# Kernel optimization log

Hardware: AMD Instinct MI355X
Metric: run time of the kernel (lower is better)

## Reference

```python
import math
import jax, jax.numpy as jnp
import numpy as np

N_HEADS = 16
NUM_BUCKETS = 32
MAX_DISTANCE = 128
ROTARY_BASE = 10000.0


def rotate_half(x):
    x1, x2 = jnp.split(x, 2, axis=-1)
    return jnp.concatenate((-x2, x1), axis=-1)


def rotary_freqs(T, dim):
    inv_freq = 1.0 / (ROTARY_BASE ** (jnp.arange(0, dim, 2, dtype=jnp.float32) / dim))
    t = jnp.arange(T, dtype=jnp.float32)
    freqs = jnp.einsum('i,j->ij', t, inv_freq)  # [T, dim/2]
    return jnp.concatenate((freqs, freqs), axis=-1)  # [T, dim]


def rel_pos_bucket_causal(rel_pos, num_buckets=NUM_BUCKETS, max_distance=MAX_DISTANCE):
    n = jnp.maximum(-rel_pos, 0)  # [T, T] int
    max_exact = num_buckets // 2
    is_small = n < max_exact
    n_safe = jnp.maximum(n, 1).astype(jnp.float32)
    val_if_large = max_exact + (
        jnp.log(n_safe / max_exact) / math.log(max_distance / max_exact) * (num_buckets - max_exact)
    ).astype(jnp.int32)
    val_if_large = jnp.minimum(val_if_large, num_buckets - 1)
    return jnp.where(is_small, n, val_if_large)


def setup_inputs() -> dict:
    key = jax.random.key(0)
    ks = jax.random.split(key, 10)
    B, T, C = 2, 2048, 1024
    s = 0.02
    return {
        'x':  jax.random.normal(ks[0], (B, T, C), dtype=jnp.float32),
        'Wq': jax.random.normal(ks[1], (C, C), dtype=jnp.float32) * s,
        'bq': jnp.zeros((C,), dtype=jnp.float32),
        'Wk': jax.random.normal(ks[2], (C, C), dtype=jnp.float32) * s,
        'bk': jnp.zeros((C,), dtype=jnp.float32),
        'Wv': jax.random.normal(ks[3], (C, C), dtype=jnp.float32) * s,
        'bv': jnp.zeros((C,), dtype=jnp.float32),
        'Wp': jax.random.normal(ks[4], (C, C), dtype=jnp.float32) * s,
        'bp': jnp.zeros((C,), dtype=jnp.float32),
        'rel_bias_table': jax.random.normal(ks[5], (NUM_BUCKETS, N_HEADS), dtype=jnp.float32) * s,
    }


def reference(x, Wq, bq, Wk, bk, Wv, bv, Wp, bp, rel_bias_table):
    B, T, C = x.shape
    H = N_HEADS
    D = C // H

    def heads(y):
        return y.reshape(B, T, H, D).transpose(0, 2, 1, 3)  # [B,H,T,D]

    q = heads(x @ Wq + bq)
    k = heads(x @ Wk + bk)
    v = heads(x @ Wv + bv)

    # rotary (use_xpos=False -> scale=1)
    freqs = rotary_freqs(T, D)  # [T, D]
    cos, sin = jnp.cos(freqs), jnp.sin(freqs)
    q = q * cos + rotate_half(q) * sin
    k = k * cos + rotate_half(k) * sin

    # relative position bias (causal, scale=1.0)
    pos = jnp.arange(T)
    rel_pos = pos[None, :] - pos[:, None]  # k_pos - q_pos
    bucket = rel_pos_bucket_causal(rel_pos)  # [T, T]
    bias = rel_bias_table[bucket]  # [T, T, H]
    bias = bias.transpose(2, 0, 1)  # [H, T, T]

    att = jnp.einsum('bhid,bhjd->bhij', q, k) + bias[None]
    att = att * (1.0 / math.sqrt(D))
    causal = pos[None, :] <= pos[:, None]  # tril mask [T, T]
    att = jnp.where(causal[None, None], att, -jnp.inf)
    att = jax.nn.softmax(att, axis=-1)

    y = jnp.einsum('bhij,bhjd->bhid', att, v)  # [B,H,T,D]
    y = y.transpose(0, 2, 1, 3).reshape(B, T, C)
    return y @ Wp + bp
```

## Files before the change

kernel.cpp:

```cpp
#include <hip/hip_runtime.h>
#include <hip/hip_bf16.h>
#include <math.h>

#define B_ 2
#define T_ 2048
#define C_ 1024
#define H_ 16
#define D_ 64
#define M_ (B_ * T_)
#define K_ 1024

#define SCALE2 0.18033688011112043f

typedef short bf16x8 __attribute__((ext_vector_type(8)));
typedef float f32x4  __attribute__((ext_vector_type(4)));
typedef unsigned int u32;

__device__ __forceinline__ float u2f(unsigned short u) {
    union { unsigned int i; float f; } v; v.i = ((unsigned int)u) << 16; return v.f;
}
__device__ __forceinline__ unsigned short f2b(float f) {
    __hip_bfloat16 h = __float2bfloat16(f);
    return *reinterpret_cast<unsigned short*>(&h);
}
__device__ __forceinline__ u32 pack_bf16_rnd(float a, float b) {
    const u32 au = __float_as_uint(a) + 0x8000u;
    const u32 bu = __float_as_uint(b) + 0x8000u;
    return __builtin_amdgcn_perm(bu, au, 0x07060302u);
}
__device__ __forceinline__ void load_lds16(const void* g, void* l) {
    __builtin_amdgcn_global_load_lds(
        (const __attribute__((address_space(1))) u32*)g,
        (__attribute__((address_space(3))) u32*)l, 16, 0, 0);
}

__global__ __launch_bounds__(256) void prep(
    const float* __restrict__ x,
    const float* __restrict__ W0, const float* __restrict__ W1,
    const float* __restrict__ W2, const float* __restrict__ W3,
    const float* __restrict__ tbl,
    unsigned short* __restrict__ xb,
    unsigned short* __restrict__ T0, unsigned short* __restrict__ T1,
    unsigned short* __restrict__ T2, unsigned short* __restrict__ T3,
    float* __restrict__ dtab, float2* __restrict__ trig)
{
    __shared__ __align__(16) unsigned short tile[64][72];
    const int bx = blockIdx.x;
    const int tid = threadIdx.x;

    if (bx < 2048) {
        const int idx = bx * 256 + tid;
        const float4 a = reinterpret_cast<const float4*>(x)[idx * 2];
        const float4 b = reinterpret_cast<const float4*>(x)[idx * 2 + 1];
        unsigned short t[8] = {f2b(a.x), f2b(a.y), f2b(a.z), f2b(a.w),
                               f2b(b.x), f2b(b.y), f2b(b.z), f2b(b.w)};
        reinterpret_cast<bf16x8*>(xb)[idx] = *reinterpret_cast<const bf16x8*>(t);
    } else if (bx < 3072) {
        const int w = bx - 2048;
        const int z = w >> 8;
        const int rem = w & 255;
        const int k0 = (rem & 15) * 64, n0 = (rem >> 4) * 64;
        const float* W = z == 0 ? W0 : z == 1 ? W1 : z == 2 ? W2 : W3;
        unsigned short* Wt = z == 0 ? T0 : z == 1 ? T1 : z == 2 ? T2 : T3;

        #pragma unroll
        for (int it = 0; it < 4; ++it) {
            const int idx = it * 256 + tid;
            const int r = idx >> 4, c = (idx & 15) * 4;
            const float4 w4 = *reinterpret_cast<const float4*>(W + (size_t)(k0 + r) * C_ + n0 + c);
            tile[r][c + 0] = f2b(w4.x); tile[r][c + 1] = f2b(w4.y);
            tile[r][c + 2] = f2b(w4.z); tile[r][c + 3] = f2b(w4.w);
        }
        __syncthreads();
        #pragma unroll
        for (int it = 0; it < 2; ++it) {
            const int idx = it * 256 + tid;
            const int nc = idx >> 3, kc = (idx & 7) * 8;
            unsigned short tmp[8];
            #pragma unroll
            for (int e = 0; e < 8; ++e) tmp[e] = tile[kc + e][nc];
            *reinterpret_cast<bf16x8*>(Wt + (size_t)(n0 + nc) * K_ + k0 + kc) =
                *reinterpret_cast<const bf16x8*>(tmp);
        }
    } else {
        const int idx = (bx - 3072) * 256 + tid;
        if (idx < H_ * T_) {
            const int h = idx >> 11, n = idx & (T_ - 1);
            int bucket;
            if (n < 16) bucket = n;
            else {
                int vb = 16 + (int)(log2f((float)n * 0.0625f) * (16.0f / 3.0f));
                bucket = vb < 31 ? vb : 31;
            }
            dtab[idx] = tbl[bucket * H_ + h] * SCALE2;
        }
        const int t = idx >> 5, j = idx & 31;
        const float inv = exp2f(-(float)j * (13.287712379549449f / 32.0f));
        const float ang = (float)t * inv;
        trig[idx] = make_float2(cosf(ang), sinf(ang));
    }
}

template<int BN>
__device__ __forceinline__ void gemm_core(
    const unsigned short* __restrict__ A, const unsigned short* __restrict__ Bt,
    const float* __restrict__ bias, const float2* __restrict__ trig,
    float rot_scale, float* __restrict__ outf,
    unsigned short* __restrict__ outb, int mode, int m0, int n0)
{
    constexpr int FN  = BN / 32;
    constexpr int BCH = BN / 64;
    constexpr int NLD = 2 + BCH;
    __shared__ __align__(16) unsigned short As0[128 * 32];
    __shared__ __align__(16) unsigned short As1[128 * 32];
    __shared__ __align__(16) unsigned short As2[128 * 32];
    __shared__ __align__(16) unsigned short Bs0[BN * 32];
    __shared__ __align__(16) unsigned short Bs1[BN * 32];
    __shared__ __align__(16) unsigned short Bs2[BN * 32];

    const int tid = threadIdx.x;
    const int wid = tid >> 6, lane = tid & 63;
    const int l16 = lane & 15, quad = lane >> 4;
    const int wm = wid >> 1, wn = wid & 1;

    f32x4 acc[4][FN];
    #pragma unroll
    for (int i = 0; i < 4; ++i)
        #pragma unroll
        for (int j = 0; j < FN; ++j) acc[i][j] = (f32x4){0.f, 0.f, 0.f, 0.f};

    auto stage = [&](unsigned short* Asb, unsigned short* Bsb, int k0) {
        #pragma unroll
        for (int it = 0; it < 2; ++it) {
            const int idx = it * 256 + tid;
            const int row = idx >> 2, ch = (idx & 3) * 8;
            load_lds16(A + (size_t)(m0 + row) * K_ + k0 + ch,
                       (char*)Asb + it * 4096 + wid * 1024);
        }
        #pragma unroll
        for (int it = 0; it < BCH; ++it) {
            const int idx = it * 256 + tid;
            const int row = idx >> 2, ch = (idx & 3) * 8;
            load_lds16(Bt + (size_t)(n0 + row) * K_ + k0 + ch,
                       (char*)Bsb + it * 4096 + wid * 1024);
        }
    };
    auto compute = [&](const unsigned short* Asb, const unsigned short* Bsb) {
        bf16x8 af[4], bf[FN];
        #pragma unroll
        for (int i = 0; i < 4; ++i)
            af[i] = *reinterpret_cast<const bf16x8*>(&Asb[(wm * 64 + i * 16 + l16) * 32 + quad * 8]);
        #pragma unroll
        for (int j = 0; j < FN; ++j)
            bf[j] = *reinterpret_cast<const bf16x8*>(&Bsb[(wn * (BN / 2) + j * 16 + l16) * 32 + quad * 8]);
        #pragma unroll
        for (int i = 0; i < 4; ++i)
            #pragma unroll
            for (int j = 0; j < FN; ++j)
                acc[i][j] = __builtin_amdgcn_mfma_f32_16x16x32_bf16(af[i], bf[j], acc[i][j], 0, 0, 0);
    };
    auto step = [&](const unsigned short* cA, const unsigned short* cB,
                    unsigned short* nA, unsigned short* nB, int kn, bool do_stage) {
        if constexpr (NLD == 4) asm volatile("s_waitcnt vmcnt(4)" ::: "memory");
        else                    asm volatile("s_waitcnt vmcnt(3)" ::: "memory");
        __builtin_amdgcn_s_barrier();
        __builtin_amdgcn_sched_barrier(0);
        if (do_stage) stage(nA, nB, kn);
        compute(cA, cB);
    };

    stage(As0, Bs0, 0);
    stage(As1, Bs1, 32);

    for (int kb = 0; kb < 30; kb += 3) {
        step(As0, Bs0, As2, Bs2, (kb + 2) * 32, true);
        step(As1, Bs1, As0, Bs0, (kb + 3) * 32, true);
        step(As2, Bs2, As1, Bs1, (kb + 4) * 32, true);
    }
    step(As0, Bs0, As2, Bs2, 0, false);
    asm volatile("s_waitcnt vmcnt(0)" ::: "memory");
    __builtin_amdgcn_s_barrier();
    __builtin_amdgcn_sched_barrier(0);
    compute(As1, Bs1);

    if (mode == 1) {
        #pragma unroll
        for (int i = 0; i < 4; ++i) {
            const int mb = m0 + wm * 64 + i * 16 + quad * 4;
            const int bb = mb >> 11, tb = mb & (T_ - 1);
            #pragma unroll
            for (int jc = 0; jc < FN / 2; ++jc) {
                const int n_lo = n0 + wn * (BN / 2) + jc * 16 + l16;
                const int h = n_lo >> 6, d = n_lo & 63;
                const float bv_lo = bias[n_lo], bv_hi = bias[n_lo + 32];
                unsigned short* po = outb + (((size_t)bb * H_ + h) * T_ + tb) * D_ + d;
                #pragma unroll
                for (int r = 0; r < 4; ++r) {
                    const float2 cs = trig[(tb + r) * 32 + d];
                    const float a = acc[i][jc][r] + bv_lo;
                    const float b = acc[i][jc + FN / 2][r] + bv_hi;
                    po[(size_t)r * D_]      = f2b((a * cs.x - b * cs.y) * rot_scale);
                    po[(size_t)r * D_ + 32] = f2b((b * cs.x + a * cs.y) * rot_scale);
                }
            }
        }
        return;
    }

    #pragma unroll
    for (int i = 0; i < 4; ++i) {
        const int mb = m0 + wm * 64 + i * 16 + quad * 4;
        #pragma unroll
        for (int j = 0; j < FN; ++j) {
            const int n = n0 + wn * (BN / 2) + j * 16 + l16;
            const float bv = bias[n];
            if (mode == 2) {
                const int bb = mb >> 11, t = mb & (T_ - 1);
                const int h = n >> 6, d = n & 63;
                uint2 w;
                w.x = pack_bf16_rnd(acc[i][j][0] + bv, acc[i][j][1] + bv);
                w.y = pack_bf16_rnd(acc[i][j][2] + bv, acc[i][j][3] + bv);
                *reinterpret_cast<uint2*>(
                    outb + (((size_t)bb * H_ + h) * D_ + d) * T_ + t) = w;
            } else {
                #pragma unroll
                for (int r = 0; r < 4; ++r)
                    outf[(size_t)(mb + r) * C_ + n] = acc[i][j][r] + bv;
            }
        }
    }
}

__global__ __launch_bounds__(256) void gemm_qkv(
    const unsigned short* __restrict__ A,
    const unsigned short* __restrict__ Wq, const unsigned short* __restrict__ Wk,
    const unsigned short* __restrict__ Wv,
    const float* __restrict__ bq, const float* __restrict__ bk,
    const float* __restrict__ bv, const float2* __restrict__ trig,
    unsigned short* __restrict__ Qo, unsigned short* __restrict__ Ko,
    unsigned short* __restrict__ Vto)
{
    const int lin = (int)blockIdx.x;
    const int g = lin & 7, slot = lin >> 3;
    const int w = g * 96 + slot;
    const int z = w >> 8, rem = w & 255;
    const int m0 = (rem >> 3) * 128, n0 = (rem & 7) * 128;

    const unsigned short* Bt = z == 0 ? Wq : z == 1 ? Wk : Wv;
    const float* bias = z == 0 ? bq : z == 1 ? bk : bv;
    unsigned short* outb = z == 0 ? Qo : z == 1 ? Ko : Vto;
    const float rs = z == 0 ? SCALE2 : 1.0f;
    gemm_core<128>(A, Bt, bias, trig, rs, nullptr, outb, z == 2 ? 2 : 1, m0, n0);
}

__global__ __launch_bounds__(256) void gemm_proj(
    const unsigned short* __restrict__ A, const unsigned short* __restrict__ Bt,
    const float* __restrict__ bias, float* __restrict__ outf)
{
    const int lin = (int)blockIdx.x;
    const int g = lin & 7, slot = lin >> 3;
    const int w = g * 64 + slot;
    const int m0 = (w >> 4) * 128, n0 = (w & 15) * 64;
    gemm_core<64>(A, Bt, bias, nullptr, 1.0f, outf, nullptr, 0, m0, n0);
}

__global__ __launch_bounds__(256) void flash_attn(
    const unsigned short* __restrict__ Q, const unsigned short* __restrict__ K,
    const unsigned short* __restrict__ Vt, const float* __restrict__ dtab,
    unsigned short* __restrict__ Y)
{
    __shared__ __align__(16) unsigned short Ks[2][64][72];
    __shared__ __align__(16) unsigned short Vs[2][64][72];
    __shared__ __align__(16) unsigned short Ps[4][16][72];
    __shared__ __align__(16) float bias_ls[64 + T_];

    const int lin = (int)(blockIdx.y * gridDim.x + blockIdx.x);
    const int bh  = lin & 31;
    const int rem = lin >> 5;
    const int h = bh & (H_ - 1), b = bh >> 4;
    const int tid = threadIdx.x;
    const int wid = tid >> 6, lane = tid & 63;
    const int l16 = lane & 15, quad = lane >> 4;
    const size_t base = (size_t)bh * T_ * D_;
    const size_t vbase = (size_t)bh * D_ * T_;

    const int qta = (rem + bh) & 15;
    const int qtb = 31 - qta;

    if (tid < 64) bias_ls[tid] = -INFINITY;
    for (int ii = tid; ii < qtb * 64 + 64; ii += 256) bias_ls[64 + ii] = dtab[h * T_ + ii];

    bf16x8 ones;
    #pragma unroll
    for (int e = 0; e < 8; ++e) ones[e] = (short)0x3F80;

    const int sr0 = tid >> 3,         sch0 = (tid & 7) * 8;
    const int sr1 = (tid + 256) >> 3, sch1 = ((tid + 256) & 7) * 8;

    bf16x8 kr[2], vr[2];
    kr[0] = *reinterpret_cast<const bf16x8*>(K + base + (size_t)sr0 * D_ + sch0);
    kr[1] = *reinterpret_cast<const bf16x8*>(K + base + (size_t)sr1 * D_ + sch1);
    vr[0] = *reinterpret_cast<const bf16x8*>(Vt + vbase + (size_t)sr0 * T_ + sch0);
    vr[1] = *reinterpret_cast<const bf16x8*>(Vt + vbase + (size_t)sr1 * T_ + sch1);
    *reinterpret_cast<bf16x8*>(&Ks[0][sr0][sch0]) = kr[0];
    *reinterpret_cast<bf16x8*>(&Ks[0][sr1][sch1]) = kr[1];
    *reinterpret_cast<bf16x8*>(&Vs[0][sr0][sch0]) = vr[0];
    *reinterpret_cast<bf16x8*>(&Vs[0][sr1][sch1]) = vr[1];
    kr[0] = *reinterpret_cast<const bf16x8*>(K + base + (size_t)(64 + sr0) * D_ + sch0);
    kr[1] = *reinterpret_cast<const bf16x8*>(K + base + (size_t)(64 + sr1) * D_ + sch1);
    vr[0] = *reinterpret_cast<const bf16x8*>(Vt + vbase + (size_t)sr0 * T_ + 64 + sch0);
    vr[1] = *reinterpret_cast<const bf16x8*>(Vt + vbase + (size_t)sr1 * T_ + 64 + sch1);
    __syncthreads();

    int t = 0;
    for (int qi = 0; qi < 2; ++qi) {
        const int qt = qi ? qta : qtb;
        const int q0 = qt * 64;
        const int arow = q0 + wid * 16 + l16;
        const int crow = q0 + wid * 16 + quad * 4;
        const int nbase = crow - l16 * 4;

        bf16x8 qf[2];
        qf[0] = *reinterpret_cast<const bf16x8*>(Q + base + (size_t)arow * D_ + quad * 8);
        qf[1] = *reinterpret_cast<const bf16x8*>(Q + base + (size_t)arow * D_ + 32 + quad * 8);

        f32x4 o[4], ol;
        #pragma unroll
        for (int c = 0; c < 4; ++c) o[c] = (f32x4){0.f, 0.f, 0.f, 0.f};
        ol = (f32x4){0.f, 0.f, 0.f, 0.f};

        for (int kt = 0; kt <= qt; ++kt, ++t) {
            const int j0 = kt * 64;
            const int cur = t & 1, nxt = cur ^ 1;

            if (t < 32) {
                *reinterpret_cast<bf16x8*>(&Ks[nxt][sr0][sch0]) = kr[0];
                *reinterpret_cast<bf16x8*>(&Ks[nxt][sr1][sch1]) = kr[1];
                *reinterpret_cast<bf16x8*>(&Vs[nxt][sr0][sch0]) = vr[0];
                *reinterpret_cast<bf16x8*>(&Vs[nxt][sr1][sch1]) = vr[1];
            }
            if (t < 31) {
                const int tn = t + 2;
                const int jn = (tn <= qtb ? tn : tn - qtb - 1) * 64;
                kr[0] = *reinterpret_cast<const bf16x8*>(K + base + (size_t)(jn + sr0) * D_ + sch0);
                kr[1] = *reinterpret_cast<const bf16x8*>(K + base + (size_t)(jn + sr1) * D_ + sch1);
                vr[0] = *reinterpret_cast<const bf16x8*>(Vt + vbase + (size_t)sr0 * T_ + jn + sch0);
                vr[1] = *reinterpret_cast<const bf16x8*>(Vt + vbase + (size_t)sr1 * T_ + jn + sch1);
            }

            const int d0 = nbase - j0;
            const f32x4 blo = *reinterpret_cast<const f32x4*>(&bias_ls[60 + d0]);
            const f32x4 bhi = *reinterpret_cast<const f32x4*>(&bias_ls[64 + d0]);

            f32x4 sc[4];
            #pragma unroll
            for (int c = 0; c < 4; ++c) {
                #pragma unroll
                for (int r = 0; r < 4; ++r)
                    sc[c][r] = (r >= c) ? bhi[r - c] : blo[4 + r - c];
            }
            __builtin_amdgcn_s_setprio(1);
            #pragma unroll
            for (int c = 0; c < 4; ++c) {
                #pragma unroll
                for (int s = 0; s < 2; ++s) {
                    bf16x8 kf = *reinterpret_cast<const bf16x8*>(
                        &Ks[cur][l16 * 4 + c][s * 32 + quad * 8]);
                    sc[c] = __builtin_amdgcn_mfma_f32_16x16x32_bf16(qf[s], kf, sc[c], 0, 0, 0);
                }
            }
            __builtin_amdgcn_s_setprio(0);

            #pragma unroll
            for (int r = 0; r < 4; ++r) {
                const float p0 = __builtin_amdgcn_exp2f(sc[0][r]);
                const float p1 = __builtin_amdgcn_exp2f(sc[1][r]);
                const float p2 = __builtin_amdgcn_exp2f(sc[2][r]);
                const float p3 = __builtin_amdgcn_exp2f(sc[3][r]);
                uint2 w;
                w.x = pack_bf16_rnd(p0, p1);
                w.y = pack_bf16_rnd(p2, p3);
                *reinterpret_cast<uint2*>(&Ps[wid][quad * 4 + r][l16 * 4]) = w;
            }

            __builtin_amdgcn_s_setprio(1);
            #pragma unroll
            for (int s = 0; s < 2; ++s) {
                bf16x8 pf = *reinterpret_cast<const bf16x8*>(&Ps[wid][l16][s * 32 + quad * 8]);
                #pragma unroll
                for (int c = 0; c < 4; ++c) {
                    bf16x8 vf = *reinterpret_cast<const bf16x8*>(&Vs[cur][c * 16 + l16][s * 32 + quad * 8]);
                    o[c] = __builtin_amdgcn_mfma_f32_16x16x32_bf16(pf, vf, o[c], 0, 0, 0);
                }
                ol = __builtin_amdgcn_mfma_f32_16x16x32_bf16(pf, ones, ol, 0, 0, 0);
            }
            __builtin_amdgcn_s_setprio(0);

            __syncthreads();
        }

        #pragma unroll
        for (int r = 0; r < 4; ++r) {
            const int i = crow + r;
            const float invl = 1.0f / ol[r];
            #pragma unroll
            for (int c = 0; c < 4; ++c)
                Y[((size_t)b * T_ + i) * C_ + h * D_ + c * 16 + l16] = f2b(o[c][r] * invl);
        }
    }
}

extern "C" void kernel_launch(void* const* d_in, const int* in_sizes, int n_in,
                              void* d_out, int out_size, void* d_ws, size_t ws_size,
                              hipStream_t stream)
{
    const float* x   = (const float*)d_in[0];
    const float* Wq  = (const float*)d_in[1];
    const float* bq  = (const float*)d_in[2];
    const float* Wk  = (const float*)d_in[3];
    const float* bk  = (const float*)d_in[4];
    const float* Wv  = (const float*)d_in[5];
    const float* bv  = (const float*)d_in[6];
    const float* Wp  = (const float*)d_in[7];
    const float* bp  = (const float*)d_in[8];
    const float* tbl = (const float*)d_in[9];
    float* out = (float*)d_out;

    const size_t n1 = (size_t)B_ * H_ * T_ * D_;
    const size_t nW = (size_t)C_ * C_;
    unsigned short* xb  = (unsigned short*)d_ws;
    unsigned short* Wqt = xb + (size_t)M_ * K_;
    unsigned short* Wkt = Wqt + nW;
    unsigned short* Wvt = Wkt + nW;
    unsigned short* Wpt = Wvt + nW;
    unsigned short* Qb  = Wpt + nW;
    unsigned short* Kb  = Qb + n1;
    unsigned short* Vtb = Kb + n1;
    unsigned short* Yb  = Vtb + n1;
    float* dtab = (float*)(Yb + n1);
    float2* trig = (float2*)(dtab + H_ * T_);

    const dim3 blk(256);

    prep<<<dim3(3328), blk, 0, stream>>>(x, Wq, Wk, Wv, Wp, tbl,
                                         xb, Wqt, Wkt, Wvt, Wpt, dtab, trig);

    gemm_qkv<<<dim3(768), blk, 0, stream>>>(
        xb, Wqt, Wkt, Wvt, bq, bk, bv, trig, Qb, Kb, Vtb);

    flash_attn<<<dim3(16, B_ * H_), blk, 0, stream>>>(Qb, Kb, Vtb, dtab, Yb);

    gemm_proj<<<dim3(512), blk, 0, stream>>>(Yb, Wpt, bp, out);
}
```

Measured before the change: 194.0 us.

## Load K/V fragments directly from global memory, one q-tile per block

The flash attention kernel stops staging K and V tiles through double-buffered shared memory and now has each wave read its MFMA operand fragments straight from global memory (relying on L2/L1 caching across the four waves). The paired-tile load balancing, where each block handled two complementary query tiles, is replaced by one query tile per block across 1024 blocks, ordered longest tile first, and occupancy is hinted with launch_bounds(256,4). This removes the LDS write/read traffic and the per-iteration block barrier. The cost is redundant global/L1 loads across waves, less coalesced fragment access, and a less even per-block workload.

```diff
diff --git a/kernel.cpp b/kernel.cpp
--- a/kernel.cpp
+++ b/kernel.cpp
@@ -264,149 +264,116 @@
     gemm_core<64>(A, Bt, bias, nullptr, 1.0f, outf, nullptr, 0, m0, n0);
 }
 
-__global__ __launch_bounds__(256) void flash_attn(
+__global__ __launch_bounds__(256, 4) void flash_attn(
     const unsigned short* __restrict__ Q, const unsigned short* __restrict__ K,
     const unsigned short* __restrict__ Vt, const float* __restrict__ dtab,
     unsigned short* __restrict__ Y)
 {
-    __shared__ __align__(16) unsigned short Ks[2][64][72];
-    __shared__ __align__(16) unsigned short Vs[2][64][72];
     __shared__ __align__(16) unsigned short Ps[4][16][72];
     __shared__ __align__(16) float bias_ls[64 + T_];
 
-    const int lin = (int)(blockIdx.y * gridDim.x + blockIdx.x);
+    const int lin = (int)blockIdx.x;
     const int bh  = lin & 31;
-    const int rem = lin >> 5;
+    const int qt  = 31 - (lin >> 5);
     const int h = bh & (H_ - 1), b = bh >> 4;
     const int tid = threadIdx.x;
     const int wid = tid >> 6, lane = tid & 63;
     const int l16 = lane & 15, quad = lane >> 4;
     const size_t base = (size_t)bh * T_ * D_;
     const size_t vbase = (size_t)bh * D_ * T_;
-
-    const int qta = (rem + bh) & 15;
-    const int qtb = 31 - qta;
+    const int q0 = qt * 64;
 
     if (tid < 64) bias_ls[tid] = -INFINITY;
-    for (int ii = tid; ii < qtb * 64 + 64; ii += 256) bias_ls[64 + ii] = dtab[h * T_ + ii];
+    for (int ii = tid; ii < q0 + 64; ii += 256) bias_ls[64 + ii] = dtab[h * T_ + ii];
+    __syncthreads();
 
     bf16x8 ones;
     #pragma unroll
     for (int e = 0; e < 8; ++e) ones[e] = (short)0x3F80;
 
-    const int sr0 = tid >> 3,         sch0 = (tid & 7) * 8;
-    const int sr1 = (tid + 256) >> 3, sch1 = ((tid + 256) & 7) * 8;
-
-    bf16x8 kr[2], vr[2];
-    kr[0] = *reinterpret_cast<const bf16x8*>(K + base + (size_t)sr0 * D_ + sch0);
-    kr[1] = *reinterpret_cast<const bf16x8*>(K + base + (size_t)sr1 * D_ + sch1);
-    vr[0] = *reinterpret_cast<const bf16x8*>(Vt + vbase + (size_t)sr0 * T_ + sch0);
-    vr[1] = *reinterpret_cast<const bf16x8*>(Vt + vbase + (size_t)sr1 * T_ + sch1);
-    *reinterpret_cast<bf16x8*>(&Ks[0][sr0][sch0]) = kr[0];
-    *reinterpret_cast<bf16x8*>(&Ks[0][sr1][sch1]) = kr[1];
-    *reinterpret_cast<bf16x8*>(&Vs[0][sr0][sch0]) = vr[0];
-    *reinterpret_cast<bf16x8*>(&Vs[0][sr1][sch1]) = vr[1];
-    kr[0] = *reinterpret_cast<const bf16x8*>(K + base + (size_t)(64 + sr0) * D_ + sch0);
-    kr[1] = *reinterpret_cast<const bf16x8*>(K + base + (size_t)(64 + sr1) * D_ + sch1);
-    vr[0] = *reinterpret_cast<const bf16x8*>(Vt + vbase + (size_t)sr0 * T_ + 64 + sch0);
-    vr[1] = *reinterpret_cast<const bf16x8*>(Vt + vbase + (size_t)sr1 * T_ + 64 + sch1);
-    __syncthreads();
-
-    int t = 0;
-    for (int qi = 0; qi < 2; ++qi) {
-        const int qt = qi ? qta : qtb;
-        const int q0 = qt * 64;
-        const int arow = q0 + wid * 16 + l16;
-        const int crow = q0 + wid * 16 + quad * 4;
-        const int nbase = crow - l16 * 4;
-
-        bf16x8 qf[2];
-        qf[0] = *reinterpret_cast<const bf16x8*>(Q + base + (size_t)arow * D_ + quad * 8);
-        qf[1] = *reinterpret_cast<const bf16x8*>(Q + base + (size_t)arow * D_ + 32 + quad * 8);
-
-        f32x4 o[4], ol;
-        #pragma unroll
-        for (int c = 0; c < 4; ++c) o[c] = (f32x4){0.f, 0.f, 0.f, 0.f};
-        ol = (f32x4){0.f, 0.f, 0.f, 0.f};
-
-        for (int kt = 0; kt <= qt; ++kt, ++t) {
-            const int j0 = kt * 64;
-            const int cur = t & 1, nxt = cur ^ 1;
-
-            if (t < 32) {
-                *reinterpret_cast<bf16x8*>(&Ks[nxt][sr0][sch0]) = kr[0];
-                *reinterpret_cast<bf16x8*>(&Ks[nxt][sr1][sch1]) = kr[1];
-                *reinterpret_cast<bf16x8*>(&Vs[nxt][sr0][sch0]) = vr[0];
-                *reinterpret_cast<bf16x8*>(&Vs[nxt][sr1][sch1]) = vr[1];
-            }
-            if (t < 31) {
-                const int tn = t + 2;
-                const int jn = (tn <= qtb ? tn : tn - qtb - 1) * 64;
-                kr[0] = *reinterpret_cast<const bf16x8*>(K + base + (size_t)(jn + sr0) * D_ + sch0);
-                kr[1] = *reinterpret_cast<const bf16x8*>(K + base + (size_t)(jn + sr1) * D_ + sch1);
-                vr[0] = *reinterpret_cast<const bf16x8*>(Vt + vbase + (size_t)sr0 * T_ + jn + sch0);
-                vr[1] = *reinterpret_cast<const bf16x8*>(Vt + vbase + (size_t)sr1 * T_ + jn + sch1);
-            }
-
-            const int d0 = nbase - j0;
-            const f32x4 blo = *reinterpret_cast<const f32x4*>(&bias_ls[60 + d0]);
-            const f32x4 bhi = *reinterpret_cast<const f32x4*>(&bias_ls[64 + d0]);
-
-            f32x4 sc[4];
-            #pragma unroll
-            for (int c = 0; c < 4; ++c) {
-                #pragma unroll
-                for (int r = 0; r < 4; ++r)
-                    sc[c][r] = (r >= c) ? bhi[r - c] : blo[4 + r - c];
-            }
-            __builtin_amdgcn_s_setprio(1);
-            #pragma unroll
-            for (int c = 0; c < 4; ++c) {
-                #pragma unroll
-                for (int s = 0; s < 2; ++s) {
-                    bf16x8 kf = *reinterpret_cast<const bf16x8*>(
-                        &Ks[cur][l16 * 4 + c][s * 32 + quad * 8]);
-                    sc[c] = __builtin_amdgcn_mfma_f32_16x16x32_bf16(qf[s], kf, sc[c], 0, 0, 0);
-                }
-            }
-            __builtin_amdgcn_s_setprio(0);
-
-            #pragma unroll
-            for (int r = 0; r < 4; ++r) {
-                const float p0 = __builtin_amdgcn_exp2f(sc[0][r]);
-                const float p1 = __builtin_amdgcn_exp2f(sc[1][r]);
-                const float p2 = __builtin_amdgcn_exp2f(sc[2][r]);
-                const float p3 = __builtin_amdgcn_exp2f(sc[3][r]);
-                uint2 w;
-                w.x = pack_bf16_rnd(p0, p1);
-                w.y = pack_bf16_rnd(p2, p3);
-                *reinterpret_cast<uint2*>(&Ps[wid][quad * 4 + r][l16 * 4]) = w;
-            }
-
-            __builtin_amdgcn_s_setprio(1);
-            #pragma unroll
-            for (int s = 0; s < 2; ++s) {
-                bf16x8 pf = *reinterpret_cast<const bf16x8*>(&Ps[wid][l16][s * 32 + quad * 8]);
-                #pragma unroll
-                for (int c = 0; c < 4; ++c) {
-                    bf16x8 vf = *reinterpret_cast<const bf16x8*>(&Vs[cur][c * 16 + l16][s * 32 + quad * 8]);
-                    o[c] = __builtin_amdgcn_mfma_f32_16x16x32_bf16(pf, vf, o[c], 0, 0, 0);
-                }
-                ol = __builtin_amdgcn_mfma_f32_16x16x32_bf16(pf, ones, ol, 0, 0, 0);
-            }
-            __builtin_amdgcn_s_setprio(0);
-
-            __syncthreads();
-        }
+    const int arow = q0 + wid * 16 + l16;
+    const int crow = q0 + wid * 16 + quad * 4;
+    const int nbase = crow - l16 * 4;
+
+    bf16x8 qf[2];
+    qf[0] = *reinterpret_cast<const bf16x8*>(Q + base + (size_t)arow * D_ + quad * 8);
+    qf[1] = *reinterpret_cast<const bf16x8*>(Q + base + (size_t)arow * D_ + 32 + quad * 8);
+
+    const unsigned short* kp = K + base + (size_t)(l16 * 4) * D_ + quad * 8;
+    const unsigned short* vp = Vt + vbase + (size_t)l16 * T_ + quad * 8;
+
+    f32x4 o[4], ol;
+    #pragma unroll
+    for (int c = 0; c < 4; ++c) o[c] = (f32x4){0.f, 0.f, 0.f, 0.f};
+    ol = (f32x4){0.f, 0.f, 0.f, 0.f};
+
+    for (int kt = 0; kt <= qt; ++kt, kp += 64 * D_, vp += 64) {
+        const int j0 = kt * 64;
+
+        bf16x8 kf[4][2];
+        #pragma unroll
+        for (int c = 0; c < 4; ++c)
+            #pragma unroll
+            for (int s = 0; s < 2; ++s)
+                kf[c][s] = *reinterpret_cast<const bf16x8*>(kp + c * D_ + s * 32);
+
+        const int d0 = nbase - j0;
+        const f32x4 blo = *reinterpret_cast<const f32x4*>(&bias_ls[60 + d0]);
+        const f32x4 bhi = *reinterpret_cast<const f32x4*>(&bias_ls[64 + d0]);
+
+        f32x4 sc[4];
+        #pragma unroll
+        for (int c = 0; c < 4; ++c) {
+            #pragma unroll
+            for (int r = 0; r < 4; ++r)
+                sc[c][r] = (r >= c) ? bhi[r - c] : blo[4 + r - c];
+        }
+        __builtin_amdgcn_s_setprio(1);
+        #pragma unroll
+        for (int c = 0; c < 4; ++c)
+            #pragma unroll
+            for (int s = 0; s < 2; ++s)
+                sc[c] = __builtin_amdgcn_mfma_f32_16x16x32_bf16(qf[s], kf[c][s], sc[c], 0, 0, 0);
+        __builtin_amdgcn_s_setprio(0);
+
+        bf16x8 vf[4][2];
+        #pragma unroll
+        for (int c = 0; c < 4; ++c)
+            #pragma unroll
+            for (int s = 0; s < 2; ++s)
+                vf[c][s] = *reinterpret_cast<const bf16x8*>(vp + (size_t)c * 16 * T_ + s * 32);
 
         #pragma unroll
         for (int r = 0; r < 4; ++r) {
-            const int i = crow + r;
-            const float invl = 1.0f / ol[r];
+            const float p0 = __builtin_amdgcn_exp2f(sc[0][r]);
+            const float p1 = __builtin_amdgcn_exp2f(sc[1][r]);
+            const float p2 = __builtin_amdgcn_exp2f(sc[2][r]);
+            const float p3 = __builtin_amdgcn_exp2f(sc[3][r]);
+            uint2 w;
+            w.x = pack_bf16_rnd(p0, p1);
+            w.y = pack_bf16_rnd(p2, p3);
+            *reinterpret_cast<uint2*>(&Ps[wid][quad * 4 + r][l16 * 4]) = w;
+        }
+
+        __builtin_amdgcn_s_setprio(1);
+        #pragma unroll
+        for (int s = 0; s < 2; ++s) {
+            bf16x8 pf = *reinterpret_cast<const bf16x8*>(&Ps[wid][l16][s * 32 + quad * 8]);
             #pragma unroll
             for (int c = 0; c < 4; ++c)
-                Y[((size_t)b * T_ + i) * C_ + h * D_ + c * 16 + l16] = f2b(o[c][r] * invl);
-        }
+                o[c] = __builtin_amdgcn_mfma_f32_16x16x32_bf16(pf, vf[c][s], o[c], 0, 0, 0);
+            ol = __builtin_amdgcn_mfma_f32_16x16x32_bf16(pf, ones, ol, 0, 0, 0);
+        }
+        __builtin_amdgcn_s_setprio(0);
+    }
+
+    #pragma unroll
+    for (int r = 0; r < 4; ++r) {
+        const int i = crow + r;
+        const float invl = 1.0f / ol[r];
+        #pragma unroll
+        for (int c = 0; c < 4; ++c)
+            Y[((size_t)b * T_ + i) * C_ + h * D_ + c * 16 + l16] = f2b(o[c][r] * invl);
     }
 }
 
@@ -448,7 +415,7 @@
     gemm_qkv<<<dim3(768), blk, 0, stream>>>(
         xb, Wqt, Wkt, Wvt, bq, bk, bv, trig, Qb, Kb, Vtb);
 
-    flash_attn<<<dim3(16, B_ * H_), blk, 0, stream>>>(Qb, Kb, Vtb, dtab, Yb);
+    flash_attn<<<dim3(1024), blk, 0, stream>>>(Qb, Kb, Vtb, dtab, Yb);
 
     gemm_proj<<<dim3(512), blk, 0, stream>>>(Yb, Wpt, bp, out);
 }
```

After: 293.4 us. +51.3%, slower.
